# Performance work log

Hardware: AMD Instinct MI355X
Metric: run time of the kernel (lower is better)

The kernel has to match this reference:

```python
import jax, jax.numpy as jnp
import numpy as np

IN_DIM, OUT_DIM, NUM, K = 512, 512, 5, 3
BATCH = 4096


def extend_grid(grid, k):
    # grid: (in_dim, num+1) -> (in_dim, num+1+2k), uniform step extension on both sides
    h = (grid[:, -1:] - grid[:, :1]) / (grid.shape[1] - 1)
    left = grid[:, :1] - h * jnp.arange(k, 0, -1, dtype=grid.dtype)
    right = grid[:, -1:] + h * jnp.arange(1, k + 1, dtype=grid.dtype)
    return jnp.concatenate([left, grid, right], axis=1)


def b_batch(x, grid, k):
    # Cox-de Boor recursion. x: (in_dim, batch), grid: (in_dim, G) extended.
    xe = x[:, None, :]            # (in, 1, B)
    g = grid[:, :, None]          # (in, G, 1)
    B = ((xe >= g[:, :-1]) & (xe < g[:, 1:])).astype(x.dtype)  # degree-0 indicators
    for p in range(1, k + 1):     # unrolled over small fixed k
        left = (xe - g[:, : -(p + 1)]) / (g[:, p:-1] - g[:, : -(p + 1)])
        right = (g[:, p + 1:] - xe) / (g[:, p + 1:] - g[:, 1:-p])
        B = left * B[:, :-1] + right * B[:, 1:]
    return B                      # (in_dim, NUM+K, batch)


def kan_forward(x, grid, weight, bias):
    batch = x.shape[0]
    xt = x.T                                            # (in, B)
    sp = b_batch(xt, extend_grid(grid, K), K)           # (in, num+k, B)
    sp = jnp.transpose(sp, (2, 1, 0))                   # (B, num+k, in)
    sb = jax.nn.silu(x)[:, None, :]                     # (B, 1, in)  base_fun branch
    gs = jnp.concatenate([sp, sb], axis=1)              # (B, num+k+1, in)
    acts = (gs * x[:, None, :]).reshape(batch, -1)      # einsum 'ijk,ik->ijk' + flatten
    return acts @ weight.T + bias                       # (B, out_dim)


def setup_inputs() -> dict:
    key = jax.random.key(0)
    k1, k2, k3 = jax.random.split(key, 3)
    x = jax.random.uniform(k1, (BATCH, IN_DIM), jnp.float32, -1.0, 1.0)
    grid = jnp.tile(jnp.linspace(-1.0, 1.0, NUM + 1, dtype=jnp.float32)[None, :], (IN_DIM, 1))
    in_multi = IN_DIM * (NUM + K + 1)
    weight = jax.random.normal(k2, (OUT_DIM, in_multi), jnp.float32) / np.sqrt(in_multi).astype(np.float32)
    bias = jax.random.normal(k3, (OUT_DIM,), jnp.float32) * 0.01
    return {"x": x, "grid": grid, "weight": weight, "bias": bias}


def reference(x, grid, weight, bias):
    return kan_forward(x, grid, weight, bias)
```

## Files before the change

kernel.cpp:

```cpp
#include <hip/hip_runtime.h>
#include <hip/hip_bf16.h>

#define IN_DIM  512
#define OUT_DIM 512
#define BATCH   4096
#define KDIM    4608
#define SPLITK  4
#define KSPLIT  1152

#define WOFF_WBF  0
#define WSZ_WBF   (OUT_DIM * KDIM * 2)
#define WOFF_PART (WOFF_WBF + WSZ_WBF)
#define WSZ_PART  (SPLITK * BATCH * OUT_DIM * 2)
#define WOFF_TBL  (WOFF_PART + WSZ_PART)

typedef __attribute__((ext_vector_type(8))) short bf16x8;
typedef __attribute__((ext_vector_type(4))) float f32x4;
typedef __attribute__((ext_vector_type(8))) _Float16 h16x8;

__device__ __forceinline__ unsigned long long pack4(float a, float b, float c, float d) {
    __hip_bfloat16 ha = __float2bfloat16(a), hb = __float2bfloat16(b),
                   hc = __float2bfloat16(c), hd = __float2bfloat16(d);
    return  (unsigned long long)*reinterpret_cast<unsigned short*>(&ha)
         | ((unsigned long long)*reinterpret_cast<unsigned short*>(&hb) << 16)
         | ((unsigned long long)*reinterpret_cast<unsigned short*>(&hc) << 32)
         | ((unsigned long long)*reinterpret_cast<unsigned short*>(&hd) << 48);
}

__device__ __forceinline__ float silux(float z) {
    return z * z / (1.0f + __expf(-z));
}

__global__ __launch_bounds__(256) void cast_w_perm(const float* __restrict__ w,
                                                   short* __restrict__ wp,
                                                   const float* __restrict__ grid,
                                                   float2* __restrict__ tbl) {
    int blk = blockIdx.x;
    if (blk == 1024) {
        for (int i = threadIdx.x; i < IN_DIM; i += 256) {
            float g0 = grid[i * 6];
            float g5 = grid[i * 6 + 5];
            tbl[i] = make_float2(g0, 5.0f / (g5 - g0));
        }
        return;
    }
    int idx = blk * 256 + threadIdx.x;
    int o = idx >> 9;
    int i = idx & 511;
    const float* wo = w + (size_t)o * KDIM;
    bf16x8 v;
#pragma unroll
    for (int j = 0; j < 8; ++j) {
        __hip_bfloat16 h = __float2bfloat16(wo[j * 512 + i]);
        v[j] = *reinterpret_cast<short*>(&h);
    }
    *reinterpret_cast<bf16x8*>(wp + (size_t)o * KDIM + i * 8) = v;
    __hip_bfloat16 h8 = __float2bfloat16(wo[8 * 512 + i]);
    wp[(size_t)o * KDIM + 4096 + i] = *reinterpret_cast<short*>(&h8);
}

#define BM 128
#define BN 256
#define BK 64

__global__ __launch_bounds__(512) void gemm_fused(const float* __restrict__ x,
                                                  const short* __restrict__ Wp,
                                                  const float2* __restrict__ tbl,
                                                  _Float16* __restrict__ part) {
    __shared__ __align__(16) short As[BM * BK];
    __shared__ __align__(16) short Ws[BN * BK];

    int l  = (blockIdx.x & 7) * 32 + (blockIdx.x >> 3);
    int sk = l >> 6;
    int bm = (l & 63) >> 1;
    int bn = l & 1;

    int tid  = threadIdx.x;
    int lane = tid & 63;
    int wid  = tid >> 6;
    int wr   = wid >> 2;
    int wc   = wid & 3;

    const short* Wb = Wp + (size_t)(bn * BN) * KDIM + sk * KSPLIT;

    f32x4 acc[4][4];
#pragma unroll
    for (int m = 0; m < 4; ++m)
#pragma unroll
        for (int n = 0; n < 4; ++n) acc[m][n] = (f32x4){0.f, 0.f, 0.f, 0.f};

    int srow = lane >> 3;
    int scol = ((lane & 7) ^ srow) * 8;

    int arow  = tid >> 2;
    int cpair = (tid & 3) * 2;
    int r7    = arow & 7;
    const float* xrow = x + (size_t)(bm * BM + arow) * IN_DIM;

    for (int kb = 0; kb < KSPLIT / BK; ++kb) {
        int k0l = kb * BK;
        int k0g = sk * KSPLIT + k0l;
        __syncthreads();

#pragma unroll
        for (int i = 0; i < 4; ++i) {
            int r0 = i * 64 + wid * 8;
            __builtin_amdgcn_global_load_lds(
                (const __attribute__((address_space(1))) void*)(Wb + (size_t)(r0 + srow) * KDIM + k0l + scol),
                (__attribute__((address_space(3))) void*)(&Ws[r0 * 64]),
                16, 0, 0);
        }

        if (k0g < 4096) {
            int i0 = k0g >> 3;
#pragma unroll
            for (int c = 0; c < 2; ++c) {
                int col8 = cpair + c;
                int ii = i0 + col8;
                float xv = xrow[ii];
                float2 t = tbl[ii];
                float ss = (xv - t.x) * t.y;
                int mi = (int)ss; mi = mi < 0 ? 0 : (mi > 4 ? 4 : mi);
                float u  = ss - (float)mi;
                float u2 = u * u, u3 = u2 * u;
                float om = 1.0f - u;
                float xb = xv * (1.0f / 6.0f);
                float b0 = om * om * om * xb;
                float b1 = (3.0f * u3 - 6.0f * u2 + 4.0f) * xb;
                float b2 = (-3.0f * u3 + 3.0f * u2 + 3.0f * u + 1.0f) * xb;
                float b3 = u3 * xb;
                unsigned long long p = pack4(b0, b1, b2, b3);
                unsigned sh = (unsigned)mi << 4;
                unsigned long long l1 = p << (sh & 63);
                unsigned long long r1 = p >> ((64u - sh) & 63);
                unsigned long long lo = (sh == 64u) ? 0ull : l1;
                unsigned long long hi = (sh == 0u) ? 0ull : ((sh == 64u) ? p : r1);
                ulonglong2 v; v.x = lo; v.y = hi;
                int slot = col8 ^ r7;
                *reinterpret_cast<ulonglong2*>(&As[arow * 64 + slot * 8]) = v;
            }
        } else {
            int ib = k0g - 4096;
#pragma unroll
            for (int c = 0; c < 2; ++c) {
                int col8 = cpair + c;
                const float* xp = xrow + ib + col8 * 8;
                float4 xa = *reinterpret_cast<const float4*>(xp);
                float4 xc = *reinterpret_cast<const float4*>(xp + 4);
                ulonglong2 v;
                v.x = pack4(silux(xa.x), silux(xa.y), silux(xa.z), silux(xa.w));
                v.y = pack4(silux(xc.x), silux(xc.y), silux(xc.z), silux(xc.w));
                int slot = col8 ^ r7;
                *reinterpret_cast<ulonglong2*>(&As[arow * 64 + slot * 8]) = v;
            }
        }
        __syncthreads();

        int g  = lane >> 4;
        int fr = lane & 15;
#pragma unroll
        for (int ks = 0; ks < 2; ++ks) {
            int kk8 = ks * 4 + g;
            bf16x8 af[4], wf[4];
#pragma unroll
            for (int m = 0; m < 4; ++m) {
                int row = wr * 64 + m * 16 + fr;
                int slot = kk8 ^ (row & 7);
                af[m] = *reinterpret_cast<const bf16x8*>(&As[row * 64 + slot * 8]);
            }
#pragma unroll
            for (int n = 0; n < 4; ++n) {
                int col = wc * 64 + n * 16 + fr;
                int slot = kk8 ^ (col & 7);
                wf[n] = *reinterpret_cast<const bf16x8*>(&Ws[col * 64 + slot * 8]);
            }
#pragma unroll
            for (int m = 0; m < 4; ++m)
#pragma unroll
                for (int n = 0; n < 4; ++n)
                    acc[m][n] = __builtin_amdgcn_mfma_f32_16x16x32_bf16(af[m], wf[n], acc[m][n], 0, 0, 0);
        }
    }

    _Float16* p = part + (size_t)sk * BATCH * OUT_DIM;
    int crow0 = bm * BM + wr * 64 + (lane >> 4) * 4;
    int ccol0 = bn * BN + wc * 64 + (lane & 15);
#pragma unroll
    for (int m = 0; m < 4; ++m)
#pragma unroll
        for (int n = 0; n < 4; ++n)
#pragma unroll
            for (int r = 0; r < 4; ++r)
                p[(size_t)(crow0 + m * 16 + r) * OUT_DIM + ccol0 + n * 16] =
                    (_Float16)acc[m][n][r];
}

__global__ __launch_bounds__(256) void reduce_out(const _Float16* __restrict__ part,
                                                  const float4* __restrict__ bias,
                                                  float4* __restrict__ out) {
    int idx = blockIdx.x * 256 + threadIdx.x;
    const size_t stride = (size_t)BATCH * OUT_DIM;
    float4 b0 = bias[(idx & 63) * 2];
    float4 b1 = bias[(idx & 63) * 2 + 1];
    float a[8] = {b0.x, b0.y, b0.z, b0.w, b1.x, b1.y, b1.z, b1.w};
#pragma unroll
    for (int s = 0; s < SPLITK; ++s) {
        h16x8 v = *reinterpret_cast<const h16x8*>(part + (size_t)s * stride + (size_t)idx * 8);
#pragma unroll
        for (int j = 0; j < 8; ++j) a[j] += (float)v[j];
    }
    out[idx * 2]     = (float4){a[0], a[1], a[2], a[3]};
    out[idx * 2 + 1] = (float4){a[4], a[5], a[6], a[7]};
}

extern "C" void kernel_launch(void* const* d_in, const int* in_sizes, int n_in,
                              void* d_out, int out_size, void* d_ws, size_t ws_size,
                              hipStream_t stream) {
    (void)in_sizes; (void)n_in; (void)out_size; (void)ws_size;
    const float* x      = (const float*)d_in[0];
    const float* grid   = (const float*)d_in[1];
    const float* weight = (const float*)d_in[2];
    const float* bias   = (const float*)d_in[3];

    char* ws = (char*)d_ws;
    short*    wbf  = (short*)(ws + WOFF_WBF);
    _Float16* part = (_Float16*)(ws + WOFF_PART);
    float2*   tbl  = (float2*)(ws + WOFF_TBL);

    cast_w_perm<<<1025, 256, 0, stream>>>(weight, wbf, grid, tbl);
    gemm_fused<<<256, 512, 0, stream>>>(x, wbf, tbl, part);
    reduce_out<<<(BATCH * OUT_DIM / 8) / 256, 256, 0, stream>>>(
        part, (const float4*)bias, (float4*)d_out);
}
```

Measured before the change: 55.92 us.

## Double-buffer LDS tiles and prefetch next K-step while computing MFMAs

Converts the fused GEMM main loop to a two-stage software pipeline. The weight tile for the next K-step is issued into a second LDS buffer and the x/table values are loaded into registers before the current MFMAs run, and the B-spline/SiLU A-tile is computed after them. The aim is to hide global load latency behind matrix math and drop one barrier per step. In exchange LDS use doubles and register pressure rises, which may lower occupancy.

```diff
diff --git a/kernel.cpp b/kernel.cpp
--- a/kernel.cpp
+++ b/kernel.cpp
@@ -7,6 +7,7 @@
 #define KDIM    4608
 #define SPLITK  4
 #define KSPLIT  1152
+#define NSTEPS  (KSPLIT / 64)
 
 #define WOFF_WBF  0
 #define WSZ_WBF   (OUT_DIM * KDIM * 2)
@@ -67,8 +68,8 @@
                                                   const short* __restrict__ Wp,
                                                   const float2* __restrict__ tbl,
                                                   _Float16* __restrict__ part) {
-    __shared__ __align__(16) short As[BM * BK];
-    __shared__ __align__(16) short Ws[BN * BK];
+    __shared__ __align__(16) short As[2][BM * BK];
+    __shared__ __align__(16) short Ws[2][BN * BK];
 
     int l  = (blockIdx.x & 7) * 32 + (blockIdx.x >> 3);
     int sk = l >> 6;
@@ -91,34 +92,46 @@
 
     int srow = lane >> 3;
     int scol = ((lane & 7) ^ srow) * 8;
-
     int arow  = tid >> 2;
     int cpair = (tid & 3) * 2;
     int r7    = arow & 7;
     const float* xrow = x + (size_t)(bm * BM + arow) * IN_DIM;
 
-    for (int kb = 0; kb < KSPLIT / BK; ++kb) {
+    float  sx0, sx1; float2 st0, st1;
+    float4 va0, vb0, va1, vb1;
+
+    auto issueW = [&](int kb, int buf) {
         int k0l = kb * BK;
-        int k0g = sk * KSPLIT + k0l;
-        __syncthreads();
-
 #pragma unroll
         for (int i = 0; i < 4; ++i) {
             int r0 = i * 64 + wid * 8;
             __builtin_amdgcn_global_load_lds(
                 (const __attribute__((address_space(1))) void*)(Wb + (size_t)(r0 + srow) * KDIM + k0l + scol),
-                (__attribute__((address_space(3))) void*)(&Ws[r0 * 64]),
+                (__attribute__((address_space(3))) void*)(&Ws[buf][r0 * 64]),
                 16, 0, 0);
         }
-
+    };
+    auto loadX = [&](int kb) {
+        int k0g = sk * KSPLIT + kb * BK;
         if (k0g < 4096) {
             int i0 = k0g >> 3;
+            sx0 = xrow[i0 + cpair];     st0 = tbl[i0 + cpair];
+            sx1 = xrow[i0 + cpair + 1]; st1 = tbl[i0 + cpair + 1];
+        } else {
+            const float* xp = xrow + (k0g - 4096) + cpair * 8;
+            va0 = *reinterpret_cast<const float4*>(xp);
+            vb0 = *reinterpret_cast<const float4*>(xp + 4);
+            va1 = *reinterpret_cast<const float4*>(xp + 8);
+            vb1 = *reinterpret_cast<const float4*>(xp + 12);
+        }
+    };
+    auto computeA = [&](int kb, int buf) {
+        int k0g = sk * KSPLIT + kb * BK;
+        if (k0g < 4096) {
 #pragma unroll
             for (int c = 0; c < 2; ++c) {
-                int col8 = cpair + c;
-                int ii = i0 + col8;
-                float xv = xrow[ii];
-                float2 t = tbl[ii];
+                float xv = c ? sx1 : sx0;
+                float2 t = c ? st1 : st0;
                 float ss = (xv - t.x) * t.y;
                 int mi = (int)ss; mi = mi < 0 ? 0 : (mi > 4 ? 4 : mi);
                 float u  = ss - (float)mi;
@@ -136,28 +149,35 @@
                 unsigned long long lo = (sh == 64u) ? 0ull : l1;
                 unsigned long long hi = (sh == 0u) ? 0ull : ((sh == 64u) ? p : r1);
                 ulonglong2 v; v.x = lo; v.y = hi;
-                int slot = col8 ^ r7;
-                *reinterpret_cast<ulonglong2*>(&As[arow * 64 + slot * 8]) = v;
+                int slot = (cpair + c) ^ r7;
+                *reinterpret_cast<ulonglong2*>(&As[buf][arow * 64 + slot * 8]) = v;
             }
         } else {
-            int ib = k0g - 4096;
-#pragma unroll
-            for (int c = 0; c < 2; ++c) {
-                int col8 = cpair + c;
-                const float* xp = xrow + ib + col8 * 8;
-                float4 xa = *reinterpret_cast<const float4*>(xp);
-                float4 xc = *reinterpret_cast<const float4*>(xp + 4);
-                ulonglong2 v;
-                v.x = pack4(silux(xa.x), silux(xa.y), silux(xa.z), silux(xa.w));
-                v.y = pack4(silux(xc.x), silux(xc.y), silux(xc.z), silux(xc.w));
-                int slot = col8 ^ r7;
-                *reinterpret_cast<ulonglong2*>(&As[arow * 64 + slot * 8]) = v;
-            }
-        }
+            ulonglong2 v;
+            v.x = pack4(silux(va0.x), silux(va0.y), silux(va0.z), silux(va0.w));
+            v.y = pack4(silux(vb0.x), silux(vb0.y), silux(vb0.z), silux(vb0.w));
+            *reinterpret_cast<ulonglong2*>(&As[buf][arow * 64 + (cpair ^ r7) * 8]) = v;
+            v.x = pack4(silux(va1.x), silux(va1.y), silux(va1.z), silux(va1.w));
+            v.y = pack4(silux(vb1.x), silux(vb1.y), silux(vb1.z), silux(vb1.w));
+            *reinterpret_cast<ulonglong2*>(&As[buf][arow * 64 + ((cpair + 1) ^ r7) * 8]) = v;
+        }
+    };
+
+    issueW(0, 0);
+    loadX(0);
+    computeA(0, 0);
+
+    int g  = lane >> 4;
+    int fr = lane & 15;
+    for (int kb = 0; kb < NSTEPS; ++kb) {
+        int cur = kb & 1;
         __syncthreads();
-
-        int g  = lane >> 4;
-        int fr = lane & 15;
+        if (kb + 1 < NSTEPS) {
+            issueW(kb + 1, cur ^ 1);
+            loadX(kb + 1);
+        }
+        const short* Ac = &As[cur][0];
+        const short* Wc = &Ws[cur][0];
 #pragma unroll
         for (int ks = 0; ks < 2; ++ks) {
             int kk8 = ks * 4 + g;
@@ -166,13 +186,13 @@
             for (int m = 0; m < 4; ++m) {
                 int row = wr * 64 + m * 16 + fr;
                 int slot = kk8 ^ (row & 7);
-                af[m] = *reinterpret_cast<const bf16x8*>(&As[row * 64 + slot * 8]);
+                af[m] = *reinterpret_cast<const bf16x8*>(&Ac[row * 64 + slot * 8]);
             }
 #pragma unroll
             for (int n = 0; n < 4; ++n) {
                 int col = wc * 64 + n * 16 + fr;
                 int slot = kk8 ^ (col & 7);
-                wf[n] = *reinterpret_cast<const bf16x8*>(&Ws[col * 64 + slot * 8]);
+                wf[n] = *reinterpret_cast<const bf16x8*>(&Wc[col * 64 + slot * 8]);
             }
 #pragma unroll
             for (int m = 0; m < 4; ++m)
@@ -180,6 +200,7 @@
                 for (int n = 0; n < 4; ++n)
                     acc[m][n] = __builtin_amdgcn_mfma_f32_16x16x32_bf16(af[m], wf[n], acc[m][n], 0, 0, 0);
         }
+        if (kb + 1 < NSTEPS) computeA(kb + 1, cur ^ 1);
     }
 
     _Float16* p = part + (size_t)sk * BATCH * OUT_DIM;
```

Measured after the change: 56.95 us. Within noise of the previous version (+1.8%).
